# Kernel tuning notes

Measured on AMD Instinct MI355X. Metric: run time of the kernel, lower is better.

## Reference

```python
import jax, jax.numpy as jnp
import numpy as np

HIDDEN = 256
HEADS = 8
HEAD_DIM = HIDDEN // HEADS
RBF_DIM = 50
EPS = 1e-5


def setup_inputs() -> dict:
    key = jax.random.key(0)
    ks = jax.random.split(key, 16)
    L, P = 1024, 2048
    s = 0.02
    inp = {
        "lig_h": jax.random.normal(ks[0], (L, HIDDEN), jnp.float32),
        "prot_h": jax.random.normal(ks[1], (P, HIDDEN), jnp.float32),
        "rbf": jax.random.uniform(ks[2], (L, P, RBF_DIM), jnp.float32),
        "L": L,
        "P": P,
        "Wq": jax.random.normal(ks[3], (HIDDEN, HIDDEN), jnp.float32) * s,
        "bq": jnp.zeros((HIDDEN,), jnp.float32),
        "Wk": jax.random.normal(ks[4], (HIDDEN, HIDDEN), jnp.float32) * s,
        "bk": jnp.zeros((HIDDEN,), jnp.float32),
        "Wv": jax.random.normal(ks[5], (HIDDEN, HIDDEN), jnp.float32) * s,
        "bv": jnp.zeros((HIDDEN,), jnp.float32),
        "Wrbf": jax.random.normal(ks[6], (RBF_DIM, HEADS), jnp.float32) * s,
        "brbf": jnp.zeros((HEADS,), jnp.float32),
        "Wo": jax.random.normal(ks[7], (HIDDEN, HIDDEN), jnp.float32) * s,
        "bo": jnp.zeros((HIDDEN,), jnp.float32),
        "gamma": jnp.ones((HIDDEN,), jnp.float32),
        "beta": jnp.zeros((HIDDEN,), jnp.float32),
    }
    return inp


def reference(lig_h, prot_h, rbf, L, P, Wq, bq, Wk, bk, Wv, bv, Wrbf, brbf, Wo, bo, gamma, beta):
    scale = float(HEAD_DIM) ** 0.5
    Q = (lig_h @ Wq + bq).reshape(L, HEADS, HEAD_DIM)
    K = (prot_h @ Wk + bk).reshape(P, HEADS, HEAD_DIM)
    V = (prot_h @ Wv + bv).reshape(P, HEADS, HEAD_DIM)
    attn = jnp.einsum('lhd,phd->lph', Q, K) / scale
    dist_bias = rbf @ Wrbf + brbf          # [L, P, H]
    attn = attn + dist_bias
    attn_weights = jax.nn.softmax(attn, axis=1)  # over P (protein) axis
    attended = jnp.einsum('lph,phd->lhd', attn_weights, V).reshape(L, HIDDEN)
    y = lig_h + attended @ Wo + bo
    mu = jnp.mean(y, axis=-1, keepdims=True)
    var = jnp.var(y, axis=-1, keepdims=True)
    lig_h_out = (y - mu) * jax.lax.rsqrt(var + EPS) * gamma + beta
    return (lig_h_out, attn_weights)
```

## Files before the change

### kernel.cpp

```cpp
#include <hip/hip_runtime.h>
#include <hip/hip_bf16.h>

#define L_SZ 1024
#define P_SZ 2048
#define HID 256
#define NH 8
#define HD 32
#define NRBF 50
#define CH 32
#define NCH 64

typedef unsigned int uint32;
typedef _Float16 half2_t __attribute__((ext_vector_type(2)));
typedef __fp16 fp16x2_t __attribute__((ext_vector_type(2)));

__constant__ float kINV_SCALE = 0.17677669529663687f;

static __device__ __forceinline__ unsigned short f2h(float f) {
    union { _Float16 h; unsigned short u; } x; x.h = (_Float16)f; return x.u;
}
static __device__ __forceinline__ float h2f(unsigned short u) {
    union { unsigned short u; _Float16 h; } x; x.u = u; return (float)x.h;
}
static __device__ __forceinline__ half2_t u2h2(uint32 u) {
    union { uint32 u; half2_t h; } x; x.u = u; return x.h;
}
static __device__ __forceinline__ half2_t pk2h(float a, float b) {
    union { fp16x2_t p; half2_t h; } x; x.p = __builtin_amdgcn_cvt_pkrtz(a, b); return x.h;
}

static __device__ __forceinline__ void g2l16(const void* g, void* l) {
    __builtin_amdgcn_global_load_lds(
        (__attribute__((address_space(1))) void*)(void*)g,
        (__attribute__((address_space(3))) void*)l, 16, 0, 0);
}
static __device__ __forceinline__ void g2l4(const void* g, void* l) {
    __builtin_amdgcn_global_load_lds(
        (__attribute__((address_space(1))) void*)(void*)g,
        (__attribute__((address_space(3))) void*)l, 4, 0, 0);
}

#define WAITV0 asm volatile("s_waitcnt vmcnt(0)" ::: "memory")
#define WAITV1 asm volatile("s_waitcnt vmcnt(1)" ::: "memory")
#define CFENCE asm volatile("" ::: "memory")

__global__ __launch_bounds__(64) void k_proj(
    const float* __restrict__ lig, const float* __restrict__ prot,
    const float* __restrict__ Wq, const float* __restrict__ bq,
    const float* __restrict__ Wk, const float* __restrict__ bk,
    const float* __restrict__ Wv, const float* __restrict__ bv,
    float* __restrict__ Qf, unsigned short* __restrict__ Kb,
    unsigned short* __restrict__ Vb)
{
    __shared__ float As[8 * HID];
    const int t = threadIdx.x;
    const int r0 = blockIdx.x * 8;

    const float* src; const float* W; const float* bias; int mode; int row0;
    if (r0 < L_SZ)            { src = lig  + (size_t)r0 * HID;               W = Wq; bias = bq; mode = 0; row0 = r0; }
    else if (r0 < L_SZ + P_SZ){ src = prot + (size_t)(r0 - L_SZ) * HID;      W = Wk; bias = bk; mode = 1; row0 = r0 - L_SZ; }
    else                      { src = prot + (size_t)(r0 - L_SZ - P_SZ)*HID; W = Wv; bias = bv; mode = 2; row0 = r0 - L_SZ - P_SZ; }

    float4* A4 = (float4*)As;
    const float4* S4 = (const float4*)src;
    #pragma unroll
    for (int j = 0; j < 8; ++j) A4[t + j * 64] = S4[t + j * 64];
    __syncthreads();

    float acc[8][4];
    #pragma unroll
    for (int r = 0; r < 8; ++r)
        #pragma unroll
        for (int c = 0; c < 4; ++c) acc[r][c] = 0.f;

    for (int k4 = 0; k4 < 64; ++k4) {
        float4 av[8];
        #pragma unroll
        for (int r = 0; r < 8; ++r) av[r] = A4[r * 64 + k4];
        #pragma unroll
        for (int kk = 0; kk < 4; ++kk) {
            const float* wr = W + (size_t)(k4 * 4 + kk) * HID + t;
            #pragma unroll
            for (int c = 0; c < 4; ++c) {
                float wv = wr[c * 64];
                #pragma unroll
                for (int r = 0; r < 8; ++r)
                    acc[r][c] += ((const float*)&av[r])[kk] * wv;
            }
        }
    }

    #pragma unroll
    for (int c = 0; c < 4; ++c) {
        const int col = t + c * 64;
        const float bb = bias[col];
        #pragma unroll
        for (int r = 0; r < 8; ++r) {
            float v = acc[r][c] + bb;
            size_t idx = (size_t)(row0 + r) * HID + col;
            if (mode == 0)      Qf[idx] = v;
            else if (mode == 1) Kb[idx] = f2h(v);
            else                Vb[idx] = f2h(v);
        }
    }
}

__global__ __launch_bounds__(256, 2) void k_attn(
    const float* __restrict__ rbf, const float* __restrict__ Qf,
    const unsigned short* __restrict__ Kb, const unsigned short* __restrict__ Vb,
    const float* __restrict__ Wrbf, const float* __restrict__ brbf,
    float* __restrict__ attn_out, float* __restrict__ att_ws)
{
    __shared__ __align__(16) char sm[78400];
    char* vBB  = sm + 32768;
    char* rbfB = sm + 65536;
    float* red = (float*)(sm + 78336);

    const int t = threadIdx.x;
    const int lane = t & 63;
    const int wv = t >> 6;
    const int r = t & 31;
    const int h = t >> 5;
    const int l = blockIdx.x;
    char* aoB = (char*)attn_out + (size_t)l * (P_SZ * NH * 4);

    auto stageKV = [&](const unsigned short* src, int c, char* dst) {
        const char* gb = (const char*)src + (size_t)c * (CH * 512);
        #pragma unroll
        for (int k = 0; k < 4; ++k) {
            int s = wv * 4 + k;
            int row = s * 2 + (lane >> 5);
            int off = ((lane & 31) ^ (row & 31)) << 4;
            g2l16(gb + row * 512 + off, dst + s * 1024);
        }
    };
    auto stageRBF = [&](int c, char* dst) {
        const char* gb = (const char*)rbf + (size_t)l * 409600 + (size_t)c * 6400;
        g2l16(gb + wv * 1024 + (lane << 4), dst + wv * 1024);
        if (wv == 0)      g2l16(gb + 4096 + (lane << 4), dst + 4096);
        else if (wv == 1) g2l16(gb + 5120 + (lane << 4), dst + 5120);
        else if (wv == 2) g2l4 (gb + 6144 + (lane << 2), dst + 6144);
    };

    half2_t wrb[25];
    #pragma unroll
    for (int j = 0; j < 25; ++j)
        wrb[j] = pk2h(Wrbf[(2 * j) * NH + h], Wrbf[(2 * j + 1) * NH + h]);
    const float bh = brbf[h];

    half2_t qp[16];
    {
        const float* qq = Qf + (size_t)l * HID + h * HD;
        #pragma unroll
        for (int n = 0; n < 16; ++n)
            qp[n] = pk2h(qq[2 * n], qq[2 * n + 1]);
    }

    stageKV(Kb, 0, sm);
    stageKV(Vb, 0, vBB);
    stageRBF(0, rbfB);

    float mx = -3.0e38f, sme = 0.f;
    float O[32];
    #pragma unroll
    for (int d = 0; d < 32; ++d) O[d] = 0.f;

    for (int c = 0; c < NCH; ++c) {
        if (c == 0) { WAITV0; } else { WAITV1; }
        __builtin_amdgcn_s_barrier();
        CFENCE;
        const int cb = c & 1;
        char* kb = sm + cb * 16384;
        char* vb = vBB + cb * 16384;
        char* rb = rbfB + cb * 6400;
        if (c + 1 < NCH) {
            stageKV(Kb, c + 1, sm + (cb ^ 1) * 16384);
            stageKV(Vb, c + 1, vBB + (cb ^ 1) * 16384);
            stageRBF(c + 1, rbfB + (cb ^ 1) * 6400);
        }
        float b0 = bh, b1 = 0.f;
        const char* rrow = rb + r * 200;
        #pragma unroll
        for (int j = 0; j < 12; ++j) {
            float2 v0 = *(const float2*)(rrow + (2 * j) * 8);
            float2 v1 = *(const float2*)(rrow + (2 * j + 1) * 8);
            b0 = __builtin_amdgcn_fdot2(pk2h(v0.x, v0.y), wrb[2 * j], b0, false);
            b1 = __builtin_amdgcn_fdot2(pk2h(v1.x, v1.y), wrb[2 * j + 1], b1, false);
        }
        {
            float2 v = *(const float2*)(rrow + 24 * 8);
            b0 = __builtin_amdgcn_fdot2(pk2h(v.x, v.y), wrb[24], b0, false);
        }
        float qk0 = 0.f, qk1 = 0.f;
        const char* krow = kb + r * 512;
        #pragma unroll
        for (int jw = 0; jw < 2; ++jw) {
            int offA = (h * 64 + jw * 16) ^ (r << 4);
            int offB = (h * 64 + (jw + 2) * 16) ^ (r << 4);
            uint4 ka = *(const uint4*)(krow + offA);
            uint4 kbv = *(const uint4*)(krow + offB);
            qk0 = __builtin_amdgcn_fdot2(u2h2(ka.x),  qp[jw * 4 + 0], qk0, false);
            qk1 = __builtin_amdgcn_fdot2(u2h2(kbv.x), qp[(jw + 2) * 4 + 0], qk1, false);
            qk0 = __builtin_amdgcn_fdot2(u2h2(ka.y),  qp[jw * 4 + 1], qk0, false);
            qk1 = __builtin_amdgcn_fdot2(u2h2(kbv.y), qp[(jw + 2) * 4 + 1], qk1, false);
            qk0 = __builtin_amdgcn_fdot2(u2h2(ka.z),  qp[jw * 4 + 2], qk0, false);
            qk1 = __builtin_amdgcn_fdot2(u2h2(kbv.z), qp[(jw + 2) * 4 + 2], qk1, false);
            qk0 = __builtin_amdgcn_fdot2(u2h2(ka.w),  qp[jw * 4 + 3], qk0, false);
            qk1 = __builtin_amdgcn_fdot2(u2h2(kbv.w), qp[(jw + 2) * 4 + 3], qk1, false);
        }
        float lg = (qk0 + qk1) * kINV_SCALE + (b0 + b1);

        if (lg > mx + 8.0f) {
            float e = __expf(mx - lg);
            sme *= e;
            #pragma unroll
            for (int d = 0; d < 32; ++d) O[d] *= e;
            mx = lg;
        }
        float w = __expf(lg - mx);
        sme += w;

        const char* vrow = vb + r * 512;
        #pragma unroll
        for (int q = 0; q < 4; ++q) {
            int off = (h * 64 + q * 16) ^ (r << 4);
            uint4 vvv = *(const uint4*)(vrow + off);
            half2_t x0 = u2h2(vvv.x), x1 = u2h2(vvv.y), x2 = u2h2(vvv.z), x3 = u2h2(vvv.w);
            O[q * 8 + 0] += w * (float)x0.x; O[q * 8 + 1] += w * (float)x0.y;
            O[q * 8 + 2] += w * (float)x1.x; O[q * 8 + 3] += w * (float)x1.y;
            O[q * 8 + 4] += w * (float)x2.x; O[q * 8 + 5] += w * (float)x2.y;
            O[q * 8 + 6] += w * (float)x3.x; O[q * 8 + 7] += w * (float)x3.y;
        }

        *(unsigned short*)(aoB + (c * CH + r) * 16 + h * 2) = f2h(lg);
    }
    WAITV0;

    float mg = mx;
    #pragma unroll
    for (int msk = 1; msk <= 16; msk <<= 1) mg = fmaxf(mg, __shfl_xor(mg, msk));
    float e = __expf(mx - mg);
    sme *= e;
    #pragma unroll
    for (int msk = 1; msk <= 16; msk <<= 1) sme += __shfl_xor(sme, msk);
    float inv = 1.0f / sme;
    if (r == 0) { red[h * 2] = mg; red[h * 2 + 1] = inv; }
    const float scl = e * inv;

    __syncthreads();

    {
        float* otr = (float*)sm;
        #pragma unroll
        for (int d = 0; d < 32; ++d)
            otr[h * 1024 + r * 32 + ((d + r) & 31)] = O[d] * scl;
        __syncthreads();
        const int hh = t >> 5, dd = t & 31;
        float a = 0.f;
        #pragma unroll
        for (int rr = 0; rr < 32; ++rr)
            a += otr[hh * 1024 + rr * 32 + ((dd + rr) & 31)];
        att_ws[(size_t)l * HID + hh * HD + dd] = a;
    }

    {
        const int hA = 2 * (t & 3);
        const float mA = red[hA * 2],     iA = red[hA * 2 + 1];
        const float mB = red[hA * 2 + 2], iB = red[hA * 2 + 3];
        for (int n = 31; n >= 0; --n) {
            int j = t + n * 256;
            uint32 a = *(const uint32*)(aoB + 4 * j);
            float w0 = __expf(h2f((unsigned short)(a & 0xffffu)) - mA) * iA;
            float w1 = __expf(h2f((unsigned short)(a >> 16))     - mB) * iB;
            __syncthreads();
            *(float2*)(aoB + 8 * (size_t)j) = make_float2(w0, w1);
        }
    }
}

__global__ __launch_bounds__(256) void k_out(
    const float* __restrict__ att, const float* __restrict__ lig,
    const float* __restrict__ Wo, const float* __restrict__ bo,
    const float* __restrict__ gamma, const float* __restrict__ beta,
    float* __restrict__ out)
{
    __shared__ float a[HID];
    __shared__ float red[8];
    const int l = blockIdx.x, t = threadIdx.x;
    if (t < 64) ((float4*)a)[t] = ((const float4*)(att + (size_t)l * HID))[t];
    __syncthreads();

    float acc = bo[t];
    for (int k4 = 0; k4 < 64; ++k4) {
        float4 av = ((float4*)a)[k4];
        const float* wr = Wo + (size_t)(k4 * 4) * HID + t;
        acc += av.x * wr[0];
        acc += av.y * wr[HID];
        acc += av.z * wr[2 * HID];
        acc += av.w * wr[3 * HID];
    }
    float y = lig[(size_t)l * HID + t] + acc;

    float s = y, sq = y * y;
    #pragma unroll
    for (int msk = 1; msk < 64; msk <<= 1) {
        s  += __shfl_xor(s, msk);
        sq += __shfl_xor(sq, msk);
    }
    const int lane = t & 63, wvi = t >> 6;
    if (lane == 0) { red[wvi * 2] = s; red[wvi * 2 + 1] = sq; }
    __syncthreads();
    float ts = red[0] + red[2] + red[4] + red[6];
    float tq = red[1] + red[3] + red[5] + red[7];
    float mu = ts * (1.0f / HID);
    float var = tq * (1.0f / HID) - mu * mu;
    out[(size_t)l * HID + t] = (y - mu) * rsqrtf(var + 1e-5f) * gamma[t] + beta[t];
}

extern "C" void kernel_launch(void* const* d_in, const int* in_sizes, int n_in,
                              void* d_out, int out_size, void* d_ws, size_t ws_size,
                              hipStream_t stream)
{
    (void)in_sizes; (void)n_in; (void)out_size; (void)ws_size;

    const float* lig   = (const float*)d_in[0];
    const float* prot  = (const float*)d_in[1];
    const float* rbf   = (const float*)d_in[2];
    const float* Wq    = (const float*)d_in[5];
    const float* bq    = (const float*)d_in[6];
    const float* Wk    = (const float*)d_in[7];
    const float* bk    = (const float*)d_in[8];
    const float* Wv    = (const float*)d_in[9];
    const float* bv    = (const float*)d_in[10];
    const float* Wrbf  = (const float*)d_in[11];
    const float* brbf  = (const float*)d_in[12];
    const float* Wo    = (const float*)d_in[13];
    const float* bo    = (const float*)d_in[14];
    const float* gamma = (const float*)d_in[15];
    const float* beta  = (const float*)d_in[16];

    float* out0 = (float*)d_out;
    float* attn = (float*)d_out + (size_t)L_SZ * HID;

    char* ws = (char*)d_ws;
    float*          Qf     = (float*)ws;
    unsigned short* Kb     = (unsigned short*)(ws + (1u << 20));
    unsigned short* Vb     = (unsigned short*)(ws + (2u << 20));
    float*          att_ws = (float*)(ws + (3u << 20));

    hipLaunchKernelGGL(k_proj, dim3((L_SZ + 2 * P_SZ) / 8), dim3(64), 0, stream,
                       lig, prot, Wq, bq, Wk, bk, Wv, bv, Qf, Kb, Vb);
    hipLaunchKernelGGL(k_attn, dim3(L_SZ), dim3(256), 0, stream,
                       rbf, Qf, Kb, Vb, Wrbf, brbf, attn, att_ws);
    hipLaunchKernelGGL(k_out, dim3(L_SZ), dim3(256), 0, stream,
                       att_ws, lig, Wo, bo, gamma, beta, out0);
}
```

Measured before the change: 273.8 us.

## Process two ligand rows per attention block to share K/V staging

The attention kernel now runs 512-thread blocks that each handle two ligand rows. The K/V chunks staged in LDS are shared by both rows, and the rbf slices of both rows are staged side by side. This halves the number of times each K/V chunk is re-read from L2/HBM per ligand row. In exchange, LDS per block grows to about 91 KB, which may limit residency to one block per CU, and the final softmax normalisation pass now loops over both rows.

```diff
diff --git a/kernel.cpp b/kernel.cpp
--- a/kernel.cpp
+++ b/kernel.cpp
@@ -105,41 +105,45 @@
     }
 }
 
-__global__ __launch_bounds__(256, 2) void k_attn(
+__global__ __launch_bounds__(512, 2) void k_attn(
     const float* __restrict__ rbf, const float* __restrict__ Qf,
     const unsigned short* __restrict__ Kb, const unsigned short* __restrict__ Vb,
     const float* __restrict__ Wrbf, const float* __restrict__ brbf,
     float* __restrict__ attn_out, float* __restrict__ att_ws)
 {
-    __shared__ __align__(16) char sm[78400];
+    __shared__ __align__(16) char sm[91264];
     char* vBB  = sm + 32768;
     char* rbfB = sm + 65536;
-    float* red = (float*)(sm + 78336);
+    float* red = (float*)(sm + 91136);
 
     const int t = threadIdx.x;
     const int lane = t & 63;
     const int wv = t >> 6;
-    const int r = t & 31;
-    const int h = t >> 5;
-    const int l = blockIdx.x;
-    char* aoB = (char*)attn_out + (size_t)l * (P_SZ * NH * 4);
+    const int r = lane & 31;
+    const int lig = wv >> 2;
+    const int h = ((wv & 3) << 1) + (lane >> 5);
+    const int l0 = blockIdx.x * 2;
+
+    char* aoB = (char*)attn_out + (size_t)(l0 + lig) * (P_SZ * NH * 4);
 
     auto stageKV = [&](const unsigned short* src, int c, char* dst) {
         const char* gb = (const char*)src + (size_t)c * (CH * 512);
         #pragma unroll
-        for (int k = 0; k < 4; ++k) {
-            int s = wv * 4 + k;
+        for (int k = 0; k < 2; ++k) {
+            int s = wv * 2 + k;
             int row = s * 2 + (lane >> 5);
             int off = ((lane & 31) ^ (row & 31)) << 4;
             g2l16(gb + row * 512 + off, dst + s * 1024);
         }
     };
-    auto stageRBF = [&](int c, char* dst) {
-        const char* gb = (const char*)rbf + (size_t)l * 409600 + (size_t)c * 6400;
-        g2l16(gb + wv * 1024 + (lane << 4), dst + wv * 1024);
-        if (wv == 0)      g2l16(gb + 4096 + (lane << 4), dst + 4096);
-        else if (wv == 1) g2l16(gb + 5120 + (lane << 4), dst + 5120);
-        else if (wv == 2) g2l4 (gb + 6144 + (lane << 2), dst + 6144);
+    auto stageRBF2 = [&](int c, char* dstBase) {
+        const int lw = wv & 1, w4 = wv >> 1;
+        const char* gb = (const char*)rbf + (size_t)(l0 + lw) * 409600 + (size_t)c * 6400;
+        char* dst = dstBase + lw * 6400;
+        g2l16(gb + w4 * 1024 + (lane << 4), dst + w4 * 1024);
+        if (w4 == 0)      g2l16(gb + 4096 + (lane << 4), dst + 4096);
+        else if (w4 == 1) g2l16(gb + 5120 + (lane << 4), dst + 5120);
+        else if (w4 == 2) g2l4 (gb + 6144 + (lane << 2), dst + 6144);
     };
 
     half2_t wrb[25];
@@ -150,7 +154,7 @@
 
     half2_t qp[16];
     {
-        const float* qq = Qf + (size_t)l * HID + h * HD;
+        const float* qq = Qf + (size_t)(l0 + lig) * HID + h * HD;
         #pragma unroll
         for (int n = 0; n < 16; ++n)
             qp[n] = pk2h(qq[2 * n], qq[2 * n + 1]);
@@ -158,7 +162,7 @@
 
     stageKV(Kb, 0, sm);
     stageKV(Vb, 0, vBB);
-    stageRBF(0, rbfB);
+    stageRBF2(0, rbfB);
 
     float mx = -3.0e38f, sme = 0.f;
     float O[32];
@@ -172,11 +176,11 @@
         const int cb = c & 1;
         char* kb = sm + cb * 16384;
         char* vb = vBB + cb * 16384;
-        char* rb = rbfB + cb * 6400;
+        char* rb = rbfB + cb * 12800 + lig * 6400;
         if (c + 1 < NCH) {
             stageKV(Kb, c + 1, sm + (cb ^ 1) * 16384);
             stageKV(Vb, c + 1, vBB + (cb ^ 1) * 16384);
-            stageRBF(c + 1, rbfB + (cb ^ 1) * 6400);
+            stageRBF2(c + 1, rbfB + (cb ^ 1) * 12800);
         }
         float b0 = bh, b1 = 0.f;
         const char* rrow = rb + r * 200;
@@ -244,36 +248,40 @@
     #pragma unroll
     for (int msk = 1; msk <= 16; msk <<= 1) sme += __shfl_xor(sme, msk);
     float inv = 1.0f / sme;
-    if (r == 0) { red[h * 2] = mg; red[h * 2 + 1] = inv; }
+    if (r == 0) { red[(lig * 8 + h) * 2] = mg; red[(lig * 8 + h) * 2 + 1] = inv; }
     const float scl = e * inv;
 
     __syncthreads();
 
     {
         float* otr = (float*)sm;
+        const int ro = ((lig * 8 + h) * 32 + r) * 32;
         #pragma unroll
         for (int d = 0; d < 32; ++d)
-            otr[h * 1024 + r * 32 + ((d + r) & 31)] = O[d] * scl;
+            otr[ro + ((d + r) & 31)] = O[d] * scl;
         __syncthreads();
-        const int hh = t >> 5, dd = t & 31;
+        const int lg2 = t >> 8, hh = (t >> 5) & 7, dd = t & 31;
         float a = 0.f;
         #pragma unroll
         for (int rr = 0; rr < 32; ++rr)
-            a += otr[hh * 1024 + rr * 32 + ((dd + rr) & 31)];
-        att_ws[(size_t)l * HID + hh * HD + dd] = a;
+            a += otr[((lg2 * 8 + hh) * 32 + rr) * 32 + ((dd + rr) & 31)];
+        att_ws[(size_t)(l0 + lg2) * HID + hh * HD + dd] = a;
     }
 
     {
         const int hA = 2 * (t & 3);
-        const float mA = red[hA * 2],     iA = red[hA * 2 + 1];
-        const float mB = red[hA * 2 + 2], iB = red[hA * 2 + 3];
-        for (int n = 31; n >= 0; --n) {
-            int j = t + n * 256;
-            uint32 a = *(const uint32*)(aoB + 4 * j);
-            float w0 = __expf(h2f((unsigned short)(a & 0xffffu)) - mA) * iA;
-            float w1 = __expf(h2f((unsigned short)(a >> 16))     - mB) * iB;
-            __syncthreads();
-            *(float2*)(aoB + 8 * (size_t)j) = make_float2(w0, w1);
+        for (int lgf = 0; lgf < 2; ++lgf) {
+            char* rg = (char*)attn_out + (size_t)(l0 + lgf) * (P_SZ * NH * 4);
+            const float mA = red[(lgf * 8 + hA) * 2],     iA = red[(lgf * 8 + hA) * 2 + 1];
+            const float mB = red[(lgf * 8 + hA + 1) * 2], iB = red[(lgf * 8 + hA + 1) * 2 + 1];
+            for (int n = 15; n >= 0; --n) {
+                int j = t + n * 512;
+                uint32 a = *(const uint32*)(rg + 4 * (size_t)j);
+                float w0 = __expf(h2f((unsigned short)(a & 0xffffu)) - mA) * iA;
+                float w1 = __expf(h2f((unsigned short)(a >> 16))     - mB) * iB;
+                __syncthreads();
+                *(float2*)(rg + 8 * (size_t)j) = make_float2(w0, w1);
+            }
         }
     }
 }
@@ -350,7 +358,7 @@
 
     hipLaunchKernelGGL(k_proj, dim3((L_SZ + 2 * P_SZ) / 8), dim3(64), 0, stream,
                        lig, prot, Wq, bq, Wk, bk, Wv, bv, Qf, Kb, Vb);
-    hipLaunchKernelGGL(k_attn, dim3(L_SZ), dim3(256), 0, stream,
+    hipLaunchKernelGGL(k_attn, dim3(L_SZ / 2), dim3(512), 0, stream,
                        rbf, Qf, Kb, Vb, Wrbf, brbf, attn, att_ws);
     hipLaunchKernelGGL(k_out, dim3(L_SZ), dim3(256), 0, stream,
                        att_ws, lig, Wo, bo, gamma, beta, out0);
```

Result: slower. 300.5 us (+9.8%).

## Split RBF distance-bias into separate kernel and shrink attention chunk tiling

Applied to the files above, without the earlier changes.

Moves the RBF·Wrbf bias computation out of the attention kernel into a new k_bias kernel that writes an fp16 [L,P,H] bias to workspace. The attention kernel now uses 16-row chunks, splits each head's dot product across two lanes with a shuffle reduction, uses less LDS and targets higher occupancy. The final per-head output reduction is done with cross-lane shuffles instead of an LDS transpose. The intent is to raise occupancy and cut per-iteration ALU in k_attn. In exchange it adds an extra launch and a 32 MB fp16 bias write plus read-back, and doubles the number of loop iterations and barriers.

```diff
diff --git a/kernel.cpp b/kernel.cpp
--- a/kernel.cpp
+++ b/kernel.cpp
@@ -7,8 +7,8 @@
 #define NH 8
 #define HD 32
 #define NRBF 50
-#define CH 32
-#define NCH 64
+#define CH 16
+#define NCH 128
 
 typedef unsigned int uint32;
 typedef _Float16 half2_t __attribute__((ext_vector_type(2)));
@@ -24,6 +24,9 @@
 }
 static __device__ __forceinline__ half2_t u2h2(uint32 u) {
     union { uint32 u; half2_t h; } x; x.u = u; return x.h;
+}
+static __device__ __forceinline__ uint32 h22u(half2_t h) {
+    union { half2_t h; uint32 u; } x; x.h = h; return x.u;
 }
 static __device__ __forceinline__ half2_t pk2h(float a, float b) {
     union { fp16x2_t p; half2_t h; } x; x.p = __builtin_amdgcn_cvt_pkrtz(a, b); return x.h;
@@ -105,134 +108,145 @@
     }
 }
 
-__global__ __launch_bounds__(256, 2) void k_attn(
-    const float* __restrict__ rbf, const float* __restrict__ Qf,
-    const unsigned short* __restrict__ Kb, const unsigned short* __restrict__ Vb,
-    const float* __restrict__ Wrbf, const float* __restrict__ brbf,
-    float* __restrict__ attn_out, float* __restrict__ att_ws)
-{
-    __shared__ __align__(16) char sm[78400];
-    char* vBB  = sm + 32768;
-    char* rbfB = sm + 65536;
-    float* red = (float*)(sm + 78336);
+__global__ __launch_bounds__(256, 4) void k_bias(
+    const float* __restrict__ rbf, const float* __restrict__ Wrbf,
+    const float* __restrict__ brbf, unsigned short* __restrict__ dbias)
+{
+    __shared__ __align__(16) char sm[7232];
+    uint32* wtab = (uint32*)(sm + 6400);
 
     const int t = threadIdx.x;
     const int lane = t & 63;
     const int wv = t >> 6;
-    const int r = t & 31;
-    const int h = t >> 5;
+    const size_t g0 = (size_t)blockIdx.x * 32;
+    const char* gb = (const char*)rbf + g0 * 200;
+
+    g2l16(gb + wv * 1024 + (lane << 4), sm + wv * 1024);
+    if (wv == 0)      g2l16(gb + 4096 + (lane << 4), sm + 4096);
+    else if (wv == 1) g2l16(gb + 5120 + (lane << 4), sm + 5120);
+    else if (wv == 2) g2l4 (gb + 6144 + (lane << 2), sm + 6144);
+
+    if (t < 200) {
+        int j = t >> 3, h = t & 7;
+        wtab[h * 25 + j] = h22u(pk2h(Wrbf[(2 * j) * NH + h], Wrbf[(2 * j + 1) * NH + h]));
+    }
+    const int h = t & 7;
+    const int r = t >> 3;
+    float b = brbf[h];
+
+    WAITV0;
+    __syncthreads();
+
+    half2_t wrb[25];
+    #pragma unroll
+    for (int j = 0; j < 25; ++j) wrb[j] = u2h2(wtab[h * 25 + j]);
+
+    const char* rrow = sm + r * 200;
+    #pragma unroll
+    for (int j = 0; j < 25; ++j) {
+        float2 v = *(const float2*)(rrow + j * 8);
+        b = __builtin_amdgcn_fdot2(pk2h(v.x, v.y), wrb[j], b, false);
+    }
+    dbias[g0 * 8 + t] = f2h(b);
+}
+
+__global__ __launch_bounds__(256, 4) void k_attn(
+    const float* __restrict__ Qf,
+    const unsigned short* __restrict__ Kb, const unsigned short* __restrict__ Vb,
+    const unsigned short* __restrict__ dbias,
+    float* __restrict__ attn_out, float* __restrict__ att_ws)
+{
+    __shared__ __align__(16) char sm[32832];
+    float* red = (float*)(sm + 32768);
+
+    const int t = threadIdx.x;
+    const int lane = t & 63;
+    const int wv = t >> 6;
+    const int hsub = lane >> 5;
+    const int rr = (lane >> 1) & 15;
+    const int half = lane & 1;
+    const int hx = wv * 2 + hsub;
     const int l = blockIdx.x;
     char* aoB = (char*)attn_out + (size_t)l * (P_SZ * NH * 4);
 
     auto stageKV = [&](const unsigned short* src, int c, char* dst) {
         const char* gb = (const char*)src + (size_t)c * (CH * 512);
         #pragma unroll
-        for (int k = 0; k < 4; ++k) {
-            int s = wv * 4 + k;
+        for (int k = 0; k < 2; ++k) {
+            int s = wv * 2 + k;
             int row = s * 2 + (lane >> 5);
-            int off = ((lane & 31) ^ (row & 31)) << 4;
+            int off = ((lane & 31) ^ (row & 7)) << 4;
             g2l16(gb + row * 512 + off, dst + s * 1024);
         }
     };
-    auto stageRBF = [&](int c, char* dst) {
-        const char* gb = (const char*)rbf + (size_t)l * 409600 + (size_t)c * 6400;
-        g2l16(gb + wv * 1024 + (lane << 4), dst + wv * 1024);
-        if (wv == 0)      g2l16(gb + 4096 + (lane << 4), dst + 4096);
-        else if (wv == 1) g2l16(gb + 5120 + (lane << 4), dst + 5120);
-        else if (wv == 2) g2l4 (gb + 6144 + (lane << 2), dst + 6144);
-    };
-
-    half2_t wrb[25];
-    #pragma unroll
-    for (int j = 0; j < 25; ++j)
-        wrb[j] = pk2h(Wrbf[(2 * j) * NH + h], Wrbf[(2 * j + 1) * NH + h]);
-    const float bh = brbf[h];
-
-    half2_t qp[16];
+
+    half2_t qp[8];
     {
-        const float* qq = Qf + (size_t)l * HID + h * HD;
-        #pragma unroll
-        for (int n = 0; n < 16; ++n)
-            qp[n] = pk2h(qq[2 * n], qq[2 * n + 1]);
+        const float* qq = Qf + (size_t)l * HID + hx * HD + half * 16;
+        #pragma unroll
+        for (int n = 0; n < 8; ++n) qp[n] = pk2h(qq[2 * n], qq[2 * n + 1]);
     }
 
     stageKV(Kb, 0, sm);
-    stageKV(Vb, 0, vBB);
-    stageRBF(0, rbfB);
+    stageKV(Vb, 0, sm + 16384);
 
     float mx = -3.0e38f, sme = 0.f;
-    float O[32];
-    #pragma unroll
-    for (int d = 0; d < 32; ++d) O[d] = 0.f;
+    float O[16];
+    #pragma unroll
+    for (int d = 0; d < 16; ++d) O[d] = 0.f;
 
     for (int c = 0; c < NCH; ++c) {
         if (c == 0) { WAITV0; } else { WAITV1; }
         __builtin_amdgcn_s_barrier();
         CFENCE;
         const int cb = c & 1;
-        char* kb = sm + cb * 16384;
-        char* vb = vBB + cb * 16384;
-        char* rb = rbfB + cb * 6400;
+        const char* kb = sm + cb * 8192;
+        const char* vb = sm + 16384 + cb * 8192;
+        unsigned short dbu = dbias[((size_t)l * P_SZ + c * CH + rr) * 8 + hx];
         if (c + 1 < NCH) {
-            stageKV(Kb, c + 1, sm + (cb ^ 1) * 16384);
-            stageKV(Vb, c + 1, vBB + (cb ^ 1) * 16384);
-            stageRBF(c + 1, rbfB + (cb ^ 1) * 6400);
-        }
-        float b0 = bh, b1 = 0.f;
-        const char* rrow = rb + r * 200;
-        #pragma unroll
-        for (int j = 0; j < 12; ++j) {
-            float2 v0 = *(const float2*)(rrow + (2 * j) * 8);
-            float2 v1 = *(const float2*)(rrow + (2 * j + 1) * 8);
-            b0 = __builtin_amdgcn_fdot2(pk2h(v0.x, v0.y), wrb[2 * j], b0, false);
-            b1 = __builtin_amdgcn_fdot2(pk2h(v1.x, v1.y), wrb[2 * j + 1], b1, false);
-        }
+            stageKV(Kb, c + 1, sm + (cb ^ 1) * 8192);
+            stageKV(Vb, c + 1, sm + 16384 + (cb ^ 1) * 8192);
+        }
+        float qk = 0.f;
         {
-            float2 v = *(const float2*)(rrow + 24 * 8);
-            b0 = __builtin_amdgcn_fdot2(pk2h(v.x, v.y), wrb[24], b0, false);
-        }
-        float qk0 = 0.f, qk1 = 0.f;
-        const char* krow = kb + r * 512;
-        #pragma unroll
-        for (int jw = 0; jw < 2; ++jw) {
-            int offA = (h * 64 + jw * 16) ^ (r << 4);
-            int offB = (h * 64 + (jw + 2) * 16) ^ (r << 4);
-            uint4 ka = *(const uint4*)(krow + offA);
-            uint4 kbv = *(const uint4*)(krow + offB);
-            qk0 = __builtin_amdgcn_fdot2(u2h2(ka.x),  qp[jw * 4 + 0], qk0, false);
-            qk1 = __builtin_amdgcn_fdot2(u2h2(kbv.x), qp[(jw + 2) * 4 + 0], qk1, false);
-            qk0 = __builtin_amdgcn_fdot2(u2h2(ka.y),  qp[jw * 4 + 1], qk0, false);
-            qk1 = __builtin_amdgcn_fdot2(u2h2(kbv.y), qp[(jw + 2) * 4 + 1], qk1, false);
-            qk0 = __builtin_amdgcn_fdot2(u2h2(ka.z),  qp[jw * 4 + 2], qk0, false);
-            qk1 = __builtin_amdgcn_fdot2(u2h2(kbv.z), qp[(jw + 2) * 4 + 2], qk1, false);
-            qk0 = __builtin_amdgcn_fdot2(u2h2(ka.w),  qp[jw * 4 + 3], qk0, false);
-            qk1 = __builtin_amdgcn_fdot2(u2h2(kbv.w), qp[(jw + 2) * 4 + 3], qk1, false);
-        }
-        float lg = (qk0 + qk1) * kINV_SCALE + (b0 + b1);
+            const char* krow = kb + rr * 512;
+            #pragma unroll
+            for (int q = 0; q < 2; ++q) {
+                int bc = hx * 64 + half * 32 + q * 16;
+                uint4 kk = *(const uint4*)(krow + (((bc >> 4) ^ (rr & 7)) << 4));
+                qk = __builtin_amdgcn_fdot2(u2h2(kk.x), qp[q * 4 + 0], qk, false);
+                qk = __builtin_amdgcn_fdot2(u2h2(kk.y), qp[q * 4 + 1], qk, false);
+                qk = __builtin_amdgcn_fdot2(u2h2(kk.z), qp[q * 4 + 2], qk, false);
+                qk = __builtin_amdgcn_fdot2(u2h2(kk.w), qp[q * 4 + 3], qk, false);
+            }
+        }
+        qk += __shfl_xor(qk, 1);
+        float lg = qk * kINV_SCALE + h2f(dbu);
 
         if (lg > mx + 8.0f) {
-            float e = __expf(mx - lg);
-            sme *= e;
+            float ee = __expf(mx - lg);
+            sme *= ee;
             #pragma unroll
-            for (int d = 0; d < 32; ++d) O[d] *= e;
+            for (int d = 0; d < 16; ++d) O[d] *= ee;
             mx = lg;
         }
         float w = __expf(lg - mx);
         sme += w;
 
-        const char* vrow = vb + r * 512;
-        #pragma unroll
-        for (int q = 0; q < 4; ++q) {
-            int off = (h * 64 + q * 16) ^ (r << 4);
-            uint4 vvv = *(const uint4*)(vrow + off);
-            half2_t x0 = u2h2(vvv.x), x1 = u2h2(vvv.y), x2 = u2h2(vvv.z), x3 = u2h2(vvv.w);
-            O[q * 8 + 0] += w * (float)x0.x; O[q * 8 + 1] += w * (float)x0.y;
-            O[q * 8 + 2] += w * (float)x1.x; O[q * 8 + 3] += w * (float)x1.y;
-            O[q * 8 + 4] += w * (float)x2.x; O[q * 8 + 5] += w * (float)x2.y;
-            O[q * 8 + 6] += w * (float)x3.x; O[q * 8 + 7] += w * (float)x3.y;
-        }
-
-        *(unsigned short*)(aoB + (c * CH + r) * 16 + h * 2) = f2h(lg);
+        {
+            const char* vrow = vb + rr * 512;
+            #pragma unroll
+            for (int q = 0; q < 2; ++q) {
+                int bc = hx * 64 + half * 32 + q * 16;
+                uint4 vv = *(const uint4*)(vrow + (((bc >> 4) ^ (rr & 7)) << 4));
+                half2_t x0 = u2h2(vv.x), x1 = u2h2(vv.y), x2 = u2h2(vv.z), x3 = u2h2(vv.w);
+                O[q * 8 + 0] += w * (float)x0.x; O[q * 8 + 1] += w * (float)x0.y;
+                O[q * 8 + 2] += w * (float)x1.x; O[q * 8 + 3] += w * (float)x1.y;
+                O[q * 8 + 4] += w * (float)x2.x; O[q * 8 + 5] += w * (float)x2.y;
+                O[q * 8 + 6] += w * (float)x3.x; O[q * 8 + 7] += w * (float)x3.y;
+            }
+        }
+        *(unsigned short*)(aoB + (c * CH + rr) * 16 + hx * 2) = f2h(lg);
     }
     WAITV0;
 
@@ -243,25 +257,24 @@
     sme *= e;
     #pragma unroll
     for (int msk = 1; msk <= 16; msk <<= 1) sme += __shfl_xor(sme, msk);
-    float inv = 1.0f / sme;
-    if (r == 0) { red[h * 2] = mg; red[h * 2 + 1] = inv; }
-    const float scl = e * inv;
-
-    __syncthreads();
-
-    {
-        float* otr = (float*)sm;
-        #pragma unroll
-        for (int d = 0; d < 32; ++d)
-            otr[h * 1024 + r * 32 + ((d + r) & 31)] = O[d] * scl;
-        __syncthreads();
-        const int hh = t >> 5, dd = t & 31;
-        float a = 0.f;
-        #pragma unroll
-        for (int rr = 0; rr < 32; ++rr)
-            a += otr[hh * 1024 + rr * 32 + ((dd + rr) & 31)];
-        att_ws[(size_t)l * HID + hh * HD + dd] = a;
-    }
+    const float invt = 2.0f / sme;
+
+    #pragma unroll
+    for (int d = 0; d < 16; ++d) O[d] *= e;
+    #pragma unroll
+    for (int msk = 2; msk <= 16; msk <<= 1) {
+        #pragma unroll
+        for (int d = 0; d < 16; ++d) O[d] += __shfl_xor(O[d], msk);
+    }
+    if (rr == 0) {
+        float* dst = att_ws + (size_t)l * HID + hx * HD + half * 16;
+        #pragma unroll
+        for (int n = 0; n < 4; ++n)
+            *(float4*)(dst + n * 4) = make_float4(O[n*4+0]*invt, O[n*4+1]*invt,
+                                                  O[n*4+2]*invt, O[n*4+3]*invt);
+        if (half == 0) { red[hx * 2] = mg; red[hx * 2 + 1] = invt; }
+    }
+    __syncthreads();
 
     {
         const int hA = 2 * (t & 3);
@@ -347,11 +360,14 @@
     unsigned short* Kb     = (unsigned short*)(ws + (1u << 20));
     unsigned short* Vb     = (unsigned short*)(ws + (2u << 20));
     float*          att_ws = (float*)(ws + (3u << 20));
+    unsigned short* dbias  = (unsigned short*)(ws + (4u << 20));
 
     hipLaunchKernelGGL(k_proj, dim3((L_SZ + 2 * P_SZ) / 8), dim3(64), 0, stream,
                        lig, prot, Wq, bq, Wk, bk, Wv, bv, Qf, Kb, Vb);
+    hipLaunchKernelGGL(k_bias, dim3((L_SZ * P_SZ) / 32), dim3(256), 0, stream,
+                       rbf, Wrbf, brbf, dbias);
     hipLaunchKernelGGL(k_attn, dim3(L_SZ), dim3(256), 0, stream,
-                       rbf, Qf, Kb, Vb, Wrbf, brbf, attn, att_ws);
+                       Qf, Kb, Vb, dbias, attn, att_ws);
     hipLaunchKernelGGL(k_out, dim3(L_SZ), dim3(256), 0, stream,
                        att_ws, lig, Wo, bo, gamma, beta, out0);
 }
```

After: 307.7 us. 12.4% more time.
